# Performance work log

Hardware: AMD Instinct MI355X
Metric: run time of the kernel (lower is better)

The kernel has to match this reference:

```python
import jax, jax.numpy as jnp
import numpy as np

B, T, N, C = 32, 12, 2048, 1
D, K, H = 10, 2, 32


def setup_inputs() -> dict:
    key = jax.random.key(0)
    ks = jax.random.split(key, 8)
    s = 0.1  # small init scale for params
    return {
        "source": jax.random.normal(ks[0], (B, T, N, C), jnp.float32),
        "node_emb": jax.random.normal(ks[1], (N, D), jnp.float32),
        "gate_W": jax.random.normal(ks[2], (D, K, C + H, 2 * H), jnp.float32) * s,
        "gate_b": jax.random.normal(ks[3], (D, 2 * H), jnp.float32) * s,
        "upd_W": jax.random.normal(ks[4], (D, K, C + H, H), jnp.float32) * s,
        "upd_b": jax.random.normal(ks[5], (D, H), jnp.float32) * s,
        "conv_W": jax.random.normal(ks[6], (T * C, 1, 1, H), jnp.float32) * s,
        "conv_b": jax.random.normal(ks[7], (T * C,), jnp.float32) * s,
    }


def reference(source, node_emb, gate_W, gate_b, upd_W, upd_b, conv_W, conv_b):
    b, t, n, c = source.shape
    h = upd_W.shape[-1]
    k = gate_W.shape[1]
    dt = source.dtype
    E = node_emb

    # Adaptive adjacency from node embeddings (time-invariant -> hoist out of scan)
    A = jax.nn.softmax(jax.nn.relu(E @ E.T), axis=1)  # [N,N]
    sup = [jnp.eye(n, dtype=dt), A]
    for i in range(2, k):
        sup.append(2.0 * (A @ sup[-1]) - sup[-2])  # Chebyshev recursion
    S = jnp.stack(sup, 0)  # [K,N,N]

    # Node-specific weights/biases from embedding pools (also time-invariant)
    Wg = jnp.einsum('nd,dkio->nkio', E, gate_W)
    bg = E @ gate_b
    Wu = jnp.einsum('nd,dkio->nkio', E, upd_W)
    bu = E @ upd_b

    def gconv(x, W, bias):  # x: [B,N,Cin] -> [B,N,Cout]
        xg = jnp.einsum('knm,bmc->bnkc', S, x)
        return jnp.einsum('bnki,nkio->bno', xg, W) + bias

    def step(state, xt):  # GRU-style AGCRN cell
        xs = jnp.concatenate([xt, state], axis=-1)
        zr = jax.nn.sigmoid(gconv(xs, Wg, bg))
        z, r = jnp.split(zr, 2, axis=-1)
        hc = jnp.tanh(gconv(jnp.concatenate([xt, z * state], axis=-1), Wu, bu))
        hnew = r * state + (1.0 - r) * hc
        return hnew, None

    h0 = jnp.zeros((b, n, h), dtype=dt)
    h_last, _ = jax.lax.scan(step, h0, jnp.swapaxes(source, 0, 1))  # carry = last state

    # end_conv: Conv2d(1, T*C, kernel=(1,H)) on [B,1,N,H] == matmul over H
    out = jnp.einsum('bnh,oh->bon', h_last, conv_W[:, 0, 0, :]) + conv_b[None, :, None]
    out = out.reshape(b, t, c, n).transpose(0, 2, 3, 1)  # [B, C, N, T]
    return out
```

## Files before the change

### kernel.cpp

```cpp
#include <hip/hip_runtime.h>
#include <hip/hip_bf16.h>
#include <math.h>


#define NNODE 2048
#define NB 32
#define NT 12
#define NH 32
#define ND 10
#define NCOL 1024
#define NCX 384
#define KPAD 96
#define GPAD 104
#define WPAD 98

#define ASCALE 256.0f
#define AINV 0.00390625f

#define KSPLIT 4
#define KCHUNK 512
#define Y1S ((size_t)NNODE * NCOL)
#define AXPS ((size_t)NNODE * NCX)

typedef _Float16 half8 __attribute__((ext_vector_type(8)));
typedef float floatx4 __attribute__((ext_vector_type(4)));

#define AS1 __attribute__((address_space(1)))
#define AS3 __attribute__((address_space(3)))
__device__ __forceinline__ void gload16(const _Float16* g, _Float16* l) {
    __builtin_amdgcn_global_load_lds((const AS1 unsigned int*)(g),
                                     (AS3 unsigned int*)(l), 16, 0, 0);
}

constexpr size_t OFF_AH  = 0;
constexpr size_t OFF_WGT = OFF_AH + 2097152u;
constexpr size_t OFF_WUT = OFF_WGT + 6291456u;
constexpr size_t OFF_BG  = OFF_WUT + 3145728u;
constexpr size_t OFF_BU  = OFF_BG + 131072u;
constexpr size_t OFF_XT  = OFF_BU + 65536u;
constexpr size_t OFF_X2T = OFF_XT + 1048576u;
constexpr size_t OFF_SXT = OFF_X2T + 1048576u;
constexpr size_t OFF_HS  = OFF_SXT + 393216u;
constexpr size_t OFF_Y   = OFF_HS + 2097152u;
constexpr size_t OFF_AXP = OFF_Y + 4194304u;
constexpr size_t OFF_R   = OFF_AXP + 1572864u;
constexpr size_t OFF_ZH  = OFF_R + 1048576u;

__global__ __launch_bounds__(256) void adj_kernel(const float* __restrict__ E,
                                                  _Float16* __restrict__ Ah) {
    __shared__ float En[ND];
    __shared__ float red[256];
    const int n = blockIdx.x;
    const int t = threadIdx.x;
    if (t < ND) En[t] = E[n * ND + t];
    __syncthreads();
    float v[8];
    float mx = 0.f;
#pragma unroll
    for (int i = 0; i < 8; ++i) {
        const int m = t + i * 256;
        float acc = 0.f;
#pragma unroll
        for (int d = 0; d < ND; ++d) acc += En[d] * E[m * ND + d];
        acc = fmaxf(acc, 0.f);
        v[i] = acc;
        mx = fmaxf(mx, acc);
    }
    red[t] = mx;
    __syncthreads();
    for (int s = 128; s > 0; s >>= 1) {
        if (t < s) red[t] = fmaxf(red[t], red[t + s]);
        __syncthreads();
    }
    mx = red[0];
    __syncthreads();
    float sum = 0.f;
#pragma unroll
    for (int i = 0; i < 8; ++i) {
        v[i] = expf(v[i] - mx);
        sum += v[i];
    }
    red[t] = sum;
    __syncthreads();
    for (int s = 128; s > 0; s >>= 1) {
        if (t < s) red[t] += red[t + s];
        __syncthreads();
    }
    const float inv = ASCALE / red[0];
#pragma unroll
    for (int i = 0; i < 8; ++i)
        Ah[(size_t)n * NNODE + t + i * 256] = (_Float16)(v[i] * inv);
}

__global__ __launch_bounds__(256) void wg_kernel(const float* __restrict__ E,
                                                 const float* __restrict__ gW,
                                                 _Float16* __restrict__ Wgt) {
    __shared__ float Es[ND];
    __shared__ _Float16 Wl[64 * WPAD];
    const int n = blockIdx.x, t = threadIdx.x;
    if (t < ND) Es[t] = E[n * ND + t];
    for (int i = t; i < 64 * WPAD / 2; i += 256) ((unsigned*)Wl)[i] = 0u;
    __syncthreads();
    for (int rem = t; rem < 4224; rem += 256) {
        float acc = 0.f;
#pragma unroll
        for (int d = 0; d < ND; ++d) acc += Es[d] * gW[d * 4224 + rem];
        const int kk = rem / 2112, r2 = rem % 2112;
        const int i = r2 >> 6, o = r2 & 63;
        Wl[o * WPAD + kk * 33 + i] = (_Float16)acc;
    }
    __syncthreads();
    const unsigned* wl = (const unsigned*)Wl;
    unsigned* dst = (unsigned*)(Wgt + (size_t)n * 6144);
    for (int idx = t; idx < 64 * 48; idx += 256) {
        const int o = idx / 48, j = idx % 48;
        dst[idx] = wl[o * (WPAD / 2) + j];
    }
}

__global__ __launch_bounds__(256) void wu_kernel(const float* __restrict__ E,
                                                 const float* __restrict__ uW,
                                                 _Float16* __restrict__ Wut) {
    __shared__ float Es[ND];
    __shared__ _Float16 Wl[32 * WPAD];
    const int n = blockIdx.x, t = threadIdx.x;
    if (t < ND) Es[t] = E[n * ND + t];
    for (int i = t; i < 32 * WPAD / 2; i += 256) ((unsigned*)Wl)[i] = 0u;
    __syncthreads();
    for (int rem = t; rem < 2112; rem += 256) {
        float acc = 0.f;
#pragma unroll
        for (int d = 0; d < ND; ++d) acc += Es[d] * uW[d * 2112 + rem];
        const int kk = rem / 1056, r2 = rem % 1056;
        const int i = r2 >> 5, o = r2 & 31;
        Wl[o * WPAD + kk * 33 + i] = (_Float16)acc;
    }
    __syncthreads();
    const unsigned* wl = (const unsigned*)Wl;
    unsigned* dst = (unsigned*)(Wut + (size_t)n * 3072);
    for (int idx = t; idx < 32 * 48; idx += 256) {
        const int o = idx / 48, j = idx % 48;
        dst[idx] = wl[o * (WPAD / 2) + j];
    }
}

__global__ __launch_bounds__(256) void bias_kernel(const float* __restrict__ E,
                                                   const float* __restrict__ gb,
                                                   const float* __restrict__ ub,
                                                   float* __restrict__ bg,
                                                   float* __restrict__ bu) {
    const int idx = blockIdx.x * 256 + threadIdx.x;
    if (idx < NNODE * 64) {
        const int n = idx >> 6, o = idx & 63;
        float acc = 0.f;
#pragma unroll
        for (int d = 0; d < ND; ++d) acc += E[n * ND + d] * gb[d * 64 + o];
        bg[idx] = acc;
    } else if (idx < NNODE * 64 + NNODE * 32) {
        const int j = idx - NNODE * 64;
        const int n = j >> 5, o = j & 31;
        float acc = 0.f;
#pragma unroll
        for (int d = 0; d < ND; ++d) acc += E[n * ND + d] * ub[d * 32 + o];
        bu[j] = acc;
    }
}

__global__ __launch_bounds__(256) void setup_kernel(const float* __restrict__ src,
                                                    _Float16* __restrict__ XT,
                                                    _Float16* __restrict__ X2T,
                                                    _Float16* __restrict__ SXT,
                                                    float* __restrict__ Hs) {
    const int idx = blockIdx.x * 256 + threadIdx.x;
    XT[idx] = (_Float16)0.f;
    X2T[idx] = (_Float16)0.f;
    Hs[idx] = 0.f;
    if (idx < NCX * NNODE) {
        const int col = idx / NNODE, n = idx % NNODE;
        const int tt = col >> 5, b = col & 31;
        SXT[idx] = (_Float16)src[((size_t)b * NT + tt) * NNODE + n];
    }
}

__global__ __launch_bounds__(256) void mm_kernel(const _Float16* __restrict__ Ah,
                                                 const _Float16* __restrict__ XT,
                                                 _Float16* __restrict__ Y, int nct) {
    __shared__ _Float16 As[128 * 32];
    __shared__ _Float16 Bs[128 * 32];
    const int t = threadIdx.x;
    const int bid = blockIdx.x;
    const int xcd = bid & 7;
    const int kz = xcd >> 1;
    const int s = (bid >> 3) * 2 + (xcd & 1);
    const int m0 = (s & 15) * 128;
    const int c0 = (s >> 4) * 128;
    const int ncols = nct << 7;
    _Float16* __restrict__ Yp = Y + (size_t)kz * NNODE * ncols;
    const int lane = t & 63;
    const int w = t >> 6;
    const int wm = (w & 1) * 64;
    const int wn = (w >> 1) * 64;
    const int lm = lane & 15;
    const int q = lane >> 4;

    const int srow = w * 32 + (lane >> 2);
    const int sq = (lane & 3) ^ ((lane >> 3) & 3);
    const _Float16* gA = Ah + (size_t)(m0 + srow) * NNODE + kz * KCHUNK + sq * 8;
    const _Float16* gB = XT + (size_t)(c0 + srow) * NNODE + kz * KCHUNK + sq * 8;
    _Float16* lA = As + w * 1024;
    _Float16* lB = Bs + w * 1024;

    const int fp = (q ^ ((lm >> 1) & 3)) * 8;

    floatx4 acc[4][4] = {};

    for (int kt = 0; kt < KCHUNK; kt += 32) {
        gload16(gA, lA);
        gload16(gA + 16 * NNODE, lA + 512);
        gload16(gB, lB);
        gload16(gB + 16 * NNODE, lB + 512);
        gA += 32;
        gB += 32;
        __syncthreads();
        half8 af[4], bf[4];
#pragma unroll
        for (int mt = 0; mt < 4; ++mt)
            af[mt] = *(const half8*)&As[(wm + mt * 16 + lm) * 32 + fp];
#pragma unroll
        for (int nt = 0; nt < 4; ++nt)
            bf[nt] = *(const half8*)&Bs[(wn + nt * 16 + lm) * 32 + fp];
#pragma unroll
        for (int mt = 0; mt < 4; ++mt)
#pragma unroll
            for (int nt = 0; nt < 4; ++nt)
                acc[mt][nt] = __builtin_amdgcn_mfma_f32_16x16x32_f16(
                    af[mt], bf[nt], acc[mt][nt], 0, 0, 0);
        __syncthreads();
    }
#pragma unroll
    for (int mt = 0; mt < 4; ++mt) {
#pragma unroll
        for (int nt = 0; nt < 4; ++nt) {
            const int row = m0 + wm + mt * 16 + q * 4;
            const int col = c0 + wn + nt * 16 + lm;
#pragma unroll
            for (int r = 0; r < 4; ++r)
                Yp[(size_t)(row + r) * ncols + col] = (_Float16)(acc[mt][nt][r] * AINV);
        }
    }
}

__global__ __launch_bounds__(256) void gate_kernel(const float* __restrict__ src, int tcur,
                                                   const _Float16* __restrict__ Y,
                                                   const _Float16* __restrict__ AXP,
                                                   const _Float16* __restrict__ Wgt,
                                                   const float* __restrict__ bg,
                                                   const float* __restrict__ Hs,
                                                   _Float16* __restrict__ X2T,
                                                   _Float16* __restrict__ zh,
                                                   _Float16* __restrict__ rbuf) {
    __shared__ _Float16 catL[4][32][GPAD];
    const int t = threadIdx.x;
    const int n0 = blockIdx.x * 4;
    {
        const int pair = t >> 1, which = t & 1;
        const int nd = pair >> 5, b = pair & 31;
        const int n1 = n0 + nd;
        if (which == 0) {
            catL[nd][b][0] = (_Float16)src[((size_t)b * NT + tcur) * NNODE + n1];
            const float* hp = Hs + (size_t)n1 * 1024 + b * 32;
#pragma unroll
            for (int i = 0; i < 32; ++i) catL[nd][b][1 + i] = (_Float16)hp[i];
#pragma unroll
            for (int i = 66; i < KPAD; i += 2) *(unsigned*)&catL[nd][b][i] = 0u;
        } else {
            const _Float16* ax = AXP + (size_t)n1 * NCX + tcur * 32 + b;
            catL[nd][b][33] = (_Float16)((float)ax[0] + (float)ax[AXPS] +
                                         (float)ax[2 * AXPS] + (float)ax[3 * AXPS]);
            const _Float16* yp = Y + (size_t)n1 * NCOL + b * 32;
#pragma unroll
            for (int i = 0; i < 32; ++i) {
                const float sv = (float)yp[i] + (float)yp[Y1S + i] +
                                 (float)yp[2 * Y1S + i] + (float)yp[3 * Y1S + i];
                catL[nd][b][34 + i] = (_Float16)sv;
            }
        }
    }
    __syncthreads();
    const int w = t >> 6, lane = t & 63, lm = lane & 15, q = lane >> 4;
    const int n = n0 + w;
    const _Float16* Wn = Wgt + (size_t)n * 6144;
    floatx4 acc[2][4] = {};
#pragma unroll
    for (int kt = 0; kt < 3; ++kt) {
        half8 af[2], bf[4];
#pragma unroll
        for (int mt = 0; mt < 2; ++mt)
            af[mt] = *(const half8*)&catL[w][mt * 16 + lm][kt * 32 + q * 8];
#pragma unroll
        for (int nt = 0; nt < 4; ++nt)
            bf[nt] = *(const half8*)(Wn + (nt * 16 + lm) * KPAD + kt * 32 + q * 8);
#pragma unroll
        for (int mt = 0; mt < 2; ++mt)
#pragma unroll
            for (int nt = 0; nt < 4; ++nt)
                acc[mt][nt] = __builtin_amdgcn_mfma_f32_16x16x32_f16(
                    af[mt], bf[nt], acc[mt][nt], 0, 0, 0);
    }
#pragma unroll
    for (int nt = 0; nt < 4; ++nt) {
        const int o = nt * 16 + lm;
        const float bias = bg[n * 64 + o];
#pragma unroll
        for (int mt = 0; mt < 2; ++mt) {
#pragma unroll
            for (int r = 0; r < 4; ++r) {
                const int b = mt * 16 + q * 4 + r;
                const float s = 1.f / (1.f + expf(-(acc[mt][nt][r] + bias)));
                if (o < 32) {
                    const float hold = Hs[(size_t)n * 1024 + b * 32 + o];
                    const _Float16 zv = (_Float16)(s * hold);
                    zh[(size_t)n * 1024 + b * 32 + o] = zv;
                    X2T[(size_t)(b * 32 + o) * NNODE + n] = zv;
                } else {
                    rbuf[(size_t)n * 1024 + b * 32 + (o - 32)] = (_Float16)s;
                }
            }
        }
    }
}

__global__ __launch_bounds__(256) void upd_kernel(const float* __restrict__ src, int tcur,
                                                  const _Float16* __restrict__ Y,
                                                  const _Float16* __restrict__ AXP,
                                                  const _Float16* __restrict__ Wut,
                                                  const float* __restrict__ bu,
                                                  const _Float16* __restrict__ zh,
                                                  const _Float16* __restrict__ rbuf,
                                                  float* __restrict__ Hs,
                                                  _Float16* __restrict__ XT) {
    __shared__ _Float16 catL[4][32][GPAD];
    const int t = threadIdx.x;
    const int n0 = blockIdx.x * 4;
    {
        const int pair = t >> 1, which = t & 1;
        const int nd = pair >> 5, b = pair & 31;
        const int n1 = n0 + nd;
        if (which == 0) {
            catL[nd][b][0] = (_Float16)src[((size_t)b * NT + tcur) * NNODE + n1];
            const _Float16* zp = zh + (size_t)n1 * 1024 + b * 32;
#pragma unroll
            for (int i = 0; i < 32; ++i) catL[nd][b][1 + i] = zp[i];
#pragma unroll
            for (int i = 66; i < KPAD; i += 2) *(unsigned*)&catL[nd][b][i] = 0u;
        } else {
            const _Float16* ax = AXP + (size_t)n1 * NCX + tcur * 32 + b;
            catL[nd][b][33] = (_Float16)((float)ax[0] + (float)ax[AXPS] +
                                         (float)ax[2 * AXPS] + (float)ax[3 * AXPS]);
            const _Float16* yp = Y + (size_t)n1 * NCOL + b * 32;
#pragma unroll
            for (int i = 0; i < 32; ++i) {
                const float sv = (float)yp[i] + (float)yp[Y1S + i] +
                                 (float)yp[2 * Y1S + i] + (float)yp[3 * Y1S + i];
                catL[nd][b][34 + i] = (_Float16)sv;
            }
        }
    }
    __syncthreads();
    const int w = t >> 6, lane = t & 63, lm = lane & 15, q = lane >> 4;
    const int n = n0 + w;
    const _Float16* Wn = Wut + (size_t)n * 3072;
    floatx4 acc[2][2] = {};
#pragma unroll
    for (int kt = 0; kt < 3; ++kt) {
        half8 af[2], bf[2];
#pragma unroll
        for (int mt = 0; mt < 2; ++mt)
            af[mt] = *(const half8*)&catL[w][mt * 16 + lm][kt * 32 + q * 8];
#pragma unroll
        for (int nt = 0; nt < 2; ++nt)
            bf[nt] = *(const half8*)(Wn + (nt * 16 + lm) * KPAD + kt * 32 + q * 8);
#pragma unroll
        for (int mt = 0; mt < 2; ++mt)
#pragma unroll
            for (int nt = 0; nt < 2; ++nt)
                acc[mt][nt] = __builtin_amdgcn_mfma_f32_16x16x32_f16(
                    af[mt], bf[nt], acc[mt][nt], 0, 0, 0);
    }
#pragma unroll
    for (int nt = 0; nt < 2; ++nt) {
        const int o = nt * 16 + lm;
        const float bias = bu[n * 32 + o];
#pragma unroll
        for (int mt = 0; mt < 2; ++mt) {
#pragma unroll
            for (int r = 0; r < 4; ++r) {
                const int b = mt * 16 + q * 4 + r;
                const float hc = tanhf(acc[mt][nt][r] + bias);
                const float rr = (float)rbuf[(size_t)n * 1024 + b * 32 + o];
                const size_t hidx = (size_t)n * 1024 + b * 32 + o;
                const float hnew = rr * Hs[hidx] + (1.f - rr) * hc;
                Hs[hidx] = hnew;
                XT[(size_t)(b * 32 + o) * NNODE + n] = (_Float16)hnew;
            }
        }
    }
}

__global__ __launch_bounds__(256) void out_kernel(const float* __restrict__ Hs,
                                                  const float* __restrict__ cw,
                                                  const float* __restrict__ cb,
                                                  float* __restrict__ out) {
    __shared__ float h[NB * NH];
    __shared__ float cws[NT * NH];
    __shared__ float cbs[NT];
    const int n = blockIdx.x;
    const int t = threadIdx.x;
    for (int i = t; i < NT * NH; i += 256) cws[i] = cw[i];
    if (t < NT) cbs[t] = cb[t];
    for (int i = t; i < NB * NH; i += 256) h[i] = Hs[(size_t)n * 1024 + i];
    __syncthreads();
    for (int p = t; p < NB * NT; p += 256) {
        const int b = p / NT, tt = p % NT;
        float acc = cbs[tt];
#pragma unroll
        for (int j = 0; j < NH; ++j) acc += h[b * NH + j] * cws[tt * NH + j];
        out[(size_t)b * NNODE * NT + (size_t)n * NT + tt] = acc;
    }
}

extern "C" void kernel_launch(void* const* d_in, const int* in_sizes, int n_in,
                              void* d_out, int out_size, void* d_ws, size_t ws_size,
                              hipStream_t stream) {
    const float* src  = (const float*)d_in[0];
    const float* E    = (const float*)d_in[1];
    const float* gW   = (const float*)d_in[2];
    const float* gb   = (const float*)d_in[3];
    const float* uW   = (const float*)d_in[4];
    const float* ub   = (const float*)d_in[5];
    const float* cw   = (const float*)d_in[6];
    const float* cb   = (const float*)d_in[7];
    float* out = (float*)d_out;

    float* ws = (float*)d_ws;
    _Float16* Ah  = (_Float16*)(ws + OFF_AH);
    _Float16* Wgt = (_Float16*)(ws + OFF_WGT);
    _Float16* Wut = (_Float16*)(ws + OFF_WUT);
    float* bg  = ws + OFF_BG;
    float* bu  = ws + OFF_BU;
    _Float16* XT  = (_Float16*)(ws + OFF_XT);
    _Float16* X2T = (_Float16*)(ws + OFF_X2T);
    _Float16* SXT = (_Float16*)(ws + OFF_SXT);
    float* Hs  = ws + OFF_HS;
    _Float16* Y   = (_Float16*)(ws + OFF_Y);
    _Float16* AXP = (_Float16*)(ws + OFF_AXP);
    _Float16* rb  = (_Float16*)(ws + OFF_R);
    _Float16* zh  = (_Float16*)(ws + OFF_ZH);

    adj_kernel<<<NNODE, 256, 0, stream>>>(E, Ah);
    wg_kernel<<<NNODE, 256, 0, stream>>>(E, gW, Wgt);
    wu_kernel<<<NNODE, 256, 0, stream>>>(E, uW, Wut);
    bias_kernel<<<(NNODE * 96 + 255) / 256, 256, 0, stream>>>(E, gb, ub, bg, bu);
    setup_kernel<<<NNODE * NCOL / 256, 256, 0, stream>>>(src, XT, X2T, SXT, Hs);

    mm_kernel<<<64 * 3, 256, 0, stream>>>(Ah, SXT, AXP, 3);

    for (int t = 0; t < NT; ++t) {
        mm_kernel<<<64 * 8, 256, 0, stream>>>(Ah, XT, Y, 8);
        gate_kernel<<<NNODE / 4, 256, 0, stream>>>(src, t, Y, AXP, Wgt, bg, Hs, X2T, zh, rb);
        mm_kernel<<<64 * 8, 256, 0, stream>>>(Ah, X2T, Y, 8);
        upd_kernel<<<NNODE / 4, 256, 0, stream>>>(src, t, Y, AXP, Wut, bu, zh, rb, Hs, XT);
    }
    out_kernel<<<NNODE, 256, 0, stream>>>(Hs, cw, cb, out);
}
```

Measured before the change: 1.167 ms.

## Fuse preprocessing kernels into one launch and deepen mm K-tile to 64

Merges the five setup kernels (adjacency softmax, gate/update weight generation, biases, buffer init) into a single block-indexed pre_kernel to cut launch overhead. The adjacency matmul kernel now stages 64-wide K tiles with an XOR swizzle over 8 chunks, halving the number of barrier/load iterations per K chunk. This doubles LDS per mm block, which may reduce occupancy.

After: 1.109 ms. 1.05x faster.

```diff
diff --git a/kernel.cpp b/kernel.cpp
--- a/kernel.cpp
+++ b/kernel.cpp
@@ -1,7 +1,6 @@
 #include <hip/hip_runtime.h>
 #include <hip/hip_bf16.h>
 #include <math.h>
-
 
 #define NNODE 2048
 #define NB 32
@@ -17,7 +16,6 @@
 #define ASCALE 256.0f
 #define AINV 0.00390625f
 
-#define KSPLIT 4
 #define KCHUNK 512
 #define Y1S ((size_t)NNODE * NCOL)
 #define AXPS ((size_t)NNODE * NCX)
@@ -46,147 +44,138 @@
 constexpr size_t OFF_R   = OFF_AXP + 1572864u;
 constexpr size_t OFF_ZH  = OFF_R + 1048576u;
 
-__global__ __launch_bounds__(256) void adj_kernel(const float* __restrict__ E,
-                                                  _Float16* __restrict__ Ah) {
-    __shared__ float En[ND];
-    __shared__ float red[256];
-    const int n = blockIdx.x;
+__global__ __launch_bounds__(256) void pre_kernel(
+    const float* __restrict__ E, const float* __restrict__ gW,
+    const float* __restrict__ uW, const float* __restrict__ gb,
+    const float* __restrict__ ub, const float* __restrict__ src,
+    _Float16* __restrict__ Ah, _Float16* __restrict__ Wgt,
+    _Float16* __restrict__ Wut, float* __restrict__ bg, float* __restrict__ bu,
+    _Float16* __restrict__ XT, _Float16* __restrict__ X2T,
+    _Float16* __restrict__ SXT, float* __restrict__ Hs) {
+    __shared__ __align__(16) float pre_f[3168];
+    const int bidg = blockIdx.x;
     const int t = threadIdx.x;
-    if (t < ND) En[t] = E[n * ND + t];
-    __syncthreads();
-    float v[8];
-    float mx = 0.f;
-#pragma unroll
-    for (int i = 0; i < 8; ++i) {
-        const int m = t + i * 256;
-        float acc = 0.f;
-#pragma unroll
-        for (int d = 0; d < ND; ++d) acc += En[d] * E[m * ND + d];
-        acc = fmaxf(acc, 0.f);
-        v[i] = acc;
-        mx = fmaxf(mx, acc);
-    }
-    red[t] = mx;
-    __syncthreads();
-    for (int s = 128; s > 0; s >>= 1) {
-        if (t < s) red[t] = fmaxf(red[t], red[t + s]);
-        __syncthreads();
-    }
-    mx = red[0];
-    __syncthreads();
-    float sum = 0.f;
-#pragma unroll
-    for (int i = 0; i < 8; ++i) {
-        v[i] = expf(v[i] - mx);
-        sum += v[i];
-    }
-    red[t] = sum;
-    __syncthreads();
-    for (int s = 128; s > 0; s >>= 1) {
-        if (t < s) red[t] += red[t + s];
-        __syncthreads();
-    }
-    const float inv = ASCALE / red[0];
-#pragma unroll
-    for (int i = 0; i < 8; ++i)
-        Ah[(size_t)n * NNODE + t + i * 256] = (_Float16)(v[i] * inv);
-}
-
-__global__ __launch_bounds__(256) void wg_kernel(const float* __restrict__ E,
-                                                 const float* __restrict__ gW,
-                                                 _Float16* __restrict__ Wgt) {
-    __shared__ float Es[ND];
-    __shared__ _Float16 Wl[64 * WPAD];
-    const int n = blockIdx.x, t = threadIdx.x;
-    if (t < ND) Es[t] = E[n * ND + t];
-    for (int i = t; i < 64 * WPAD / 2; i += 256) ((unsigned*)Wl)[i] = 0u;
-    __syncthreads();
-    for (int rem = t; rem < 4224; rem += 256) {
-        float acc = 0.f;
-#pragma unroll
-        for (int d = 0; d < ND; ++d) acc += Es[d] * gW[d * 4224 + rem];
-        const int kk = rem / 2112, r2 = rem % 2112;
-        const int i = r2 >> 6, o = r2 & 63;
-        Wl[o * WPAD + kk * 33 + i] = (_Float16)acc;
-    }
-    __syncthreads();
-    const unsigned* wl = (const unsigned*)Wl;
-    unsigned* dst = (unsigned*)(Wgt + (size_t)n * 6144);
-    for (int idx = t; idx < 64 * 48; idx += 256) {
-        const int o = idx / 48, j = idx % 48;
-        dst[idx] = wl[o * (WPAD / 2) + j];
-    }
-}
-
-__global__ __launch_bounds__(256) void wu_kernel(const float* __restrict__ E,
-                                                 const float* __restrict__ uW,
-                                                 _Float16* __restrict__ Wut) {
-    __shared__ float Es[ND];
-    __shared__ _Float16 Wl[32 * WPAD];
-    const int n = blockIdx.x, t = threadIdx.x;
-    if (t < ND) Es[t] = E[n * ND + t];
-    for (int i = t; i < 32 * WPAD / 2; i += 256) ((unsigned*)Wl)[i] = 0u;
-    __syncthreads();
-    for (int rem = t; rem < 2112; rem += 256) {
-        float acc = 0.f;
-#pragma unroll
-        for (int d = 0; d < ND; ++d) acc += Es[d] * uW[d * 2112 + rem];
-        const int kk = rem / 1056, r2 = rem % 1056;
-        const int i = r2 >> 5, o = r2 & 31;
-        Wl[o * WPAD + kk * 33 + i] = (_Float16)acc;
-    }
-    __syncthreads();
-    const unsigned* wl = (const unsigned*)Wl;
-    unsigned* dst = (unsigned*)(Wut + (size_t)n * 3072);
-    for (int idx = t; idx < 32 * 48; idx += 256) {
-        const int o = idx / 48, j = idx % 48;
-        dst[idx] = wl[o * (WPAD / 2) + j];
-    }
-}
-
-__global__ __launch_bounds__(256) void bias_kernel(const float* __restrict__ E,
-                                                   const float* __restrict__ gb,
-                                                   const float* __restrict__ ub,
-                                                   float* __restrict__ bg,
-                                                   float* __restrict__ bu) {
-    const int idx = blockIdx.x * 256 + threadIdx.x;
-    if (idx < NNODE * 64) {
-        const int n = idx >> 6, o = idx & 63;
-        float acc = 0.f;
-#pragma unroll
-        for (int d = 0; d < ND; ++d) acc += E[n * ND + d] * gb[d * 64 + o];
-        bg[idx] = acc;
-    } else if (idx < NNODE * 64 + NNODE * 32) {
-        const int j = idx - NNODE * 64;
-        const int n = j >> 5, o = j & 31;
-        float acc = 0.f;
-#pragma unroll
-        for (int d = 0; d < ND; ++d) acc += E[n * ND + d] * ub[d * 32 + o];
-        bu[j] = acc;
-    }
-}
-
-__global__ __launch_bounds__(256) void setup_kernel(const float* __restrict__ src,
-                                                    _Float16* __restrict__ XT,
-                                                    _Float16* __restrict__ X2T,
-                                                    _Float16* __restrict__ SXT,
-                                                    float* __restrict__ Hs) {
-    const int idx = blockIdx.x * 256 + threadIdx.x;
-    XT[idx] = (_Float16)0.f;
-    X2T[idx] = (_Float16)0.f;
-    Hs[idx] = 0.f;
-    if (idx < NCX * NNODE) {
-        const int col = idx / NNODE, n = idx % NNODE;
-        const int tt = col >> 5, b = col & 31;
-        SXT[idx] = (_Float16)src[((size_t)b * NT + tt) * NNODE + n];
+
+    if (bidg < 2048) {
+        float* En = pre_f;
+        float* red = pre_f + 16;
+        const int n = bidg;
+        if (t < ND) En[t] = E[n * ND + t];
+        __syncthreads();
+        float v[8];
+        float mx = 0.f;
+#pragma unroll
+        for (int i = 0; i < 8; ++i) {
+            const int m = t + i * 256;
+            float acc = 0.f;
+#pragma unroll
+            for (int d = 0; d < ND; ++d) acc += En[d] * E[m * ND + d];
+            acc = fmaxf(acc, 0.f);
+            v[i] = acc;
+            mx = fmaxf(mx, acc);
+        }
+        red[t] = mx;
+        __syncthreads();
+        for (int s = 128; s > 0; s >>= 1) {
+            if (t < s) red[t] = fmaxf(red[t], red[t + s]);
+            __syncthreads();
+        }
+        mx = red[0];
+        __syncthreads();
+        float sum = 0.f;
+#pragma unroll
+        for (int i = 0; i < 8; ++i) {
+            v[i] = expf(v[i] - mx);
+            sum += v[i];
+        }
+        red[t] = sum;
+        __syncthreads();
+        for (int s = 128; s > 0; s >>= 1) {
+            if (t < s) red[t] += red[t + s];
+            __syncthreads();
+        }
+        const float inv = ASCALE / red[0];
+#pragma unroll
+        for (int i = 0; i < 8; ++i)
+            Ah[(size_t)n * NNODE + t + i * 256] = (_Float16)(v[i] * inv);
+    } else if (bidg < 4096) {
+        float* Es = pre_f;
+        _Float16* Wl = (_Float16*)(pre_f + 16);
+        const int n = bidg - 2048;
+        if (t < ND) Es[t] = E[n * ND + t];
+        for (int i = t; i < 64 * WPAD / 2; i += 256) ((unsigned*)Wl)[i] = 0u;
+        __syncthreads();
+        for (int rem = t; rem < 4224; rem += 256) {
+            float acc = 0.f;
+#pragma unroll
+            for (int d = 0; d < ND; ++d) acc += Es[d] * gW[d * 4224 + rem];
+            const int kk = rem / 2112, r2 = rem % 2112;
+            const int i = r2 >> 6, o = r2 & 63;
+            Wl[o * WPAD + kk * 33 + i] = (_Float16)acc;
+        }
+        __syncthreads();
+        const unsigned* wl = (const unsigned*)Wl;
+        unsigned* dst = (unsigned*)(Wgt + (size_t)n * 6144);
+        for (int idx = t; idx < 64 * 48; idx += 256) {
+            const int o = idx / 48, j = idx % 48;
+            dst[idx] = wl[o * (WPAD / 2) + j];
+        }
+    } else if (bidg < 6144) {
+        float* Es = pre_f;
+        _Float16* Wl = (_Float16*)(pre_f + 16);
+        const int n = bidg - 4096;
+        if (t < ND) Es[t] = E[n * ND + t];
+        for (int i = t; i < 32 * WPAD / 2; i += 256) ((unsigned*)Wl)[i] = 0u;
+        __syncthreads();
+        for (int rem = t; rem < 2112; rem += 256) {
+            float acc = 0.f;
+#pragma unroll
+            for (int d = 0; d < ND; ++d) acc += Es[d] * uW[d * 2112 + rem];
+            const int kk = rem / 1056, r2 = rem % 1056;
+            const int i = r2 >> 5, o = r2 & 31;
+            Wl[o * WPAD + kk * 33 + i] = (_Float16)acc;
+        }
+        __syncthreads();
+        const unsigned* wl = (const unsigned*)Wl;
+        unsigned* dst = (unsigned*)(Wut + (size_t)n * 3072);
+        for (int idx = t; idx < 32 * 48; idx += 256) {
+            const int o = idx / 48, j = idx % 48;
+            dst[idx] = wl[o * (WPAD / 2) + j];
+        }
+    } else if (bidg < 6912) {
+        const int idx = (bidg - 6144) * 256 + t;
+        if (idx < NNODE * 64) {
+            const int n = idx >> 6, o = idx & 63;
+            float acc = 0.f;
+#pragma unroll
+            for (int d = 0; d < ND; ++d) acc += E[n * ND + d] * gb[d * 64 + o];
+            bg[idx] = acc;
+        } else {
+            const int j = idx - NNODE * 64;
+            const int n = j >> 5, o = j & 31;
+            float acc = 0.f;
+#pragma unroll
+            for (int d = 0; d < ND; ++d) acc += E[n * ND + d] * ub[d * 32 + o];
+            bu[j] = acc;
+        }
+    } else {
+        const int idx = (bidg - 6912) * 256 + t;
+        XT[idx] = (_Float16)0.f;
+        X2T[idx] = (_Float16)0.f;
+        Hs[idx] = 0.f;
+        if (idx < NCX * NNODE) {
+            const int col = idx >> 11, n = idx & 2047;
+            const int tt = col >> 5, b = col & 31;
+            SXT[idx] = (_Float16)src[((size_t)b * NT + tt) * NNODE + n];
+        }
     }
 }
 
 __global__ __launch_bounds__(256) void mm_kernel(const _Float16* __restrict__ Ah,
                                                  const _Float16* __restrict__ XT,
                                                  _Float16* __restrict__ Y, int nct) {
-    __shared__ _Float16 As[128 * 32];
-    __shared__ _Float16 Bs[128 * 32];
+    __shared__ _Float16 As[128 * 64];
+    __shared__ _Float16 Bs[128 * 64];
     const int t = threadIdx.x;
     const int bid = blockIdx.x;
     const int xcd = bid & 7;
@@ -203,38 +192,41 @@
     const int lm = lane & 15;
     const int q = lane >> 4;
 
-    const int srow = w * 32 + (lane >> 2);
-    const int sq = (lane & 3) ^ ((lane >> 3) & 3);
-    const _Float16* gA = Ah + (size_t)(m0 + srow) * NNODE + kz * KCHUNK + sq * 8;
-    const _Float16* gB = XT + (size_t)(c0 + srow) * NNODE + kz * KCHUNK + sq * 8;
-    _Float16* lA = As + w * 1024;
-    _Float16* lB = Bs + w * 1024;
-
-    const int fp = (q ^ ((lm >> 1) & 3)) * 8;
+    const int srow = w * 32 + (lane >> 3);
+    const int sc = ((lane & 7) ^ (lane >> 3)) * 8;
+    const _Float16* gA = Ah + (size_t)(m0 + srow) * NNODE + kz * KCHUNK + sc;
+    const _Float16* gB = XT + (size_t)(c0 + srow) * NNODE + kz * KCHUNK + sc;
+    _Float16* lA = As + w * 2048;
+    _Float16* lB = Bs + w * 2048;
 
     floatx4 acc[4][4] = {};
 
-    for (int kt = 0; kt < KCHUNK; kt += 32) {
-        gload16(gA, lA);
-        gload16(gA + 16 * NNODE, lA + 512);
-        gload16(gB, lB);
-        gload16(gB + 16 * NNODE, lB + 512);
-        gA += 32;
-        gB += 32;
-        __syncthreads();
-        half8 af[4], bf[4];
-#pragma unroll
-        for (int mt = 0; mt < 4; ++mt)
-            af[mt] = *(const half8*)&As[(wm + mt * 16 + lm) * 32 + fp];
-#pragma unroll
-        for (int nt = 0; nt < 4; ++nt)
-            bf[nt] = *(const half8*)&Bs[(wn + nt * 16 + lm) * 32 + fp];
-#pragma unroll
-        for (int mt = 0; mt < 4; ++mt)
+    for (int kt = 0; kt < KCHUNK; kt += 64) {
+#pragma unroll
+        for (int j = 0; j < 4; ++j) {
+            gload16(gA + (size_t)j * 8 * NNODE, lA + j * 512);
+            gload16(gB + (size_t)j * 8 * NNODE, lB + j * 512);
+        }
+        gA += 64;
+        gB += 64;
+        __syncthreads();
+#pragma unroll
+        for (int ks = 0; ks < 2; ++ks) {
+            const int pc = ((ks * 4 + q) ^ (lm & 7)) * 8;
+            half8 af[4], bf[4];
+#pragma unroll
+            for (int mt = 0; mt < 4; ++mt)
+                af[mt] = *(const half8*)&As[(wm + mt * 16 + lm) * 64 + pc];
 #pragma unroll
             for (int nt = 0; nt < 4; ++nt)
-                acc[mt][nt] = __builtin_amdgcn_mfma_f32_16x16x32_f16(
-                    af[mt], bf[nt], acc[mt][nt], 0, 0, 0);
+                bf[nt] = *(const half8*)&Bs[(wn + nt * 16 + lm) * 64 + pc];
+#pragma unroll
+            for (int mt = 0; mt < 4; ++mt)
+#pragma unroll
+                for (int nt = 0; nt < 4; ++nt)
+                    acc[mt][nt] = __builtin_amdgcn_mfma_f32_16x16x32_f16(
+                        af[mt], bf[nt], acc[mt][nt], 0, 0, 0);
+        }
         __syncthreads();
     }
 #pragma unroll
@@ -249,6 +241,8 @@
         }
     }
 }
+
+#define CAT(nd, b, i) cat[((nd) * 32 + (b)) * GPAD + (i)]
 
 __global__ __launch_bounds__(256) void gate_kernel(const float* __restrict__ src, int tcur,
                                                    const _Float16* __restrict__ Y,
@@ -259,7 +253,7 @@
                                                    _Float16* __restrict__ X2T,
                                                    _Float16* __restrict__ zh,
                                                    _Float16* __restrict__ rbuf) {
-    __shared__ _Float16 catL[4][32][GPAD];
+    __shared__ __align__(16) _Float16 cat[4 * 32 * GPAD];
     const int t = threadIdx.x;
     const int n0 = blockIdx.x * 4;
     {
@@ -267,22 +261,22 @@
         const int nd = pair >> 5, b = pair & 31;
         const int n1 = n0 + nd;
         if (which == 0) {
-            catL[nd][b][0] = (_Float16)src[((size_t)b * NT + tcur) * NNODE + n1];
+            CAT(nd, b, 0) = (_Float16)src[((size_t)b * NT + tcur) * NNODE + n1];
             const float* hp = Hs + (size_t)n1 * 1024 + b * 32;
 #pragma unroll
-            for (int i = 0; i < 32; ++i) catL[nd][b][1 + i] = (_Float16)hp[i];
-#pragma unroll
-            for (int i = 66; i < KPAD; i += 2) *(unsigned*)&catL[nd][b][i] = 0u;
+            for (int i = 0; i < 32; ++i) CAT(nd, b, 1 + i) = (_Float16)hp[i];
+#pragma unroll
+            for (int i = 66; i < KPAD; i += 2) *(unsigned*)&CAT(nd, b, i) = 0u;
         } else {
             const _Float16* ax = AXP + (size_t)n1 * NCX + tcur * 32 + b;
-            catL[nd][b][33] = (_Float16)((float)ax[0] + (float)ax[AXPS] +
-                                         (float)ax[2 * AXPS] + (float)ax[3 * AXPS]);
+            CAT(nd, b, 33) = (_Float16)((float)ax[0] + (float)ax[AXPS] +
+                                        (float)ax[2 * AXPS] + (float)ax[3 * AXPS]);
             const _Float16* yp = Y + (size_t)n1 * NCOL + b * 32;
 #pragma unroll
             for (int i = 0; i < 32; ++i) {
                 const float sv = (float)yp[i] + (float)yp[Y1S + i] +
                                  (float)yp[2 * Y1S + i] + (float)yp[3 * Y1S + i];
-                catL[nd][b][34 + i] = (_Float16)sv;
+                CAT(nd, b, 34 + i) = (_Float16)sv;
             }
         }
     }
@@ -296,7 +290,7 @@
         half8 af[2], bf[4];
 #pragma unroll
         for (int mt = 0; mt < 2; ++mt)
-            af[mt] = *(const half8*)&catL[w][mt * 16 + lm][kt * 32 + q * 8];
+            af[mt] = *(const half8*)&CAT(w, mt * 16 + lm, kt * 32 + q * 8);
 #pragma unroll
         for (int nt = 0; nt < 4; ++nt)
             bf[nt] = *(const half8*)(Wn + (nt * 16 + lm) * KPAD + kt * 32 + q * 8);
@@ -339,7 +333,7 @@
                                                   const _Float16* __restrict__ rbuf,
                                                   float* __restrict__ Hs,
                                                   _Float16* __restrict__ XT) {
-    __shared__ _Float16 catL[4][32][GPAD];
+    __shared__ __align__(16) _Float16 cat[4 * 32 * GPAD];
     const int t = threadIdx.x;
     const int n0 = blockIdx.x * 4;
     {
@@ -347,22 +341,22 @@
         const int nd = pair >> 5, b = pair & 31;
         const int n1 = n0 + nd;
         if (which == 0) {
-            catL[nd][b][0] = (_Float16)src[((size_t)b * NT + tcur) * NNODE + n1];
+            CAT(nd, b, 0) = (_Float16)src[((size_t)b * NT + tcur) * NNODE + n1];
             const _Float16* zp = zh + (size_t)n1 * 1024 + b * 32;
 #pragma unroll
-            for (int i = 0; i < 32; ++i) catL[nd][b][1 + i] = zp[i];
-#pragma unroll
-            for (int i = 66; i < KPAD; i += 2) *(unsigned*)&catL[nd][b][i] = 0u;
+            for (int i = 0; i < 32; ++i) CAT(nd, b, 1 + i) = zp[i];
+#pragma unroll
+            for (int i = 66; i < KPAD; i += 2) *(unsigned*)&CAT(nd, b, i) = 0u;
         } else {
             const _Float16* ax = AXP + (size_t)n1 * NCX + tcur * 32 + b;
-            catL[nd][b][33] = (_Float16)((float)ax[0] + (float)ax[AXPS] +
-                                         (float)ax[2 * AXPS] + (float)ax[3 * AXPS]);
+            CAT(nd, b, 33) = (_Float16)((float)ax[0] + (float)ax[AXPS] +
+                                        (float)ax[2 * AXPS] + (float)ax[3 * AXPS]);
             const _Float16* yp = Y + (size_t)n1 * NCOL + b * 32;
 #pragma unroll
             for (int i = 0; i < 32; ++i) {
                 const float sv = (float)yp[i] + (float)yp[Y1S + i] +
                                  (float)yp[2 * Y1S + i] + (float)yp[3 * Y1S + i];
-                catL[nd][b][34 + i] = (_Float16)sv;
+                CAT(nd, b, 34 + i) = (_Float16)sv;
             }
         }
     }
@@ -376,7 +370,7 @@
         half8 af[2], bf[2];
 #pragma unroll
         for (int mt = 0; mt < 2; ++mt)
-            af[mt] = *(const half8*)&catL[w][mt * 16 + lm][kt * 32 + q * 8];
+            af[mt] = *(const half8*)&CAT(w, mt * 16 + lm, kt * 32 + q * 8);
 #pragma unroll
         for (int nt = 0; nt < 2; ++nt)
             bf[nt] = *(const half8*)(Wn + (nt * 16 + lm) * KPAD + kt * 32 + q * 8);
@@ -457,11 +451,8 @@
     _Float16* rb  = (_Float16*)(ws + OFF_R);
     _Float16* zh  = (_Float16*)(ws + OFF_ZH);
 
-    adj_kernel<<<NNODE, 256, 0, stream>>>(E, Ah);
-    wg_kernel<<<NNODE, 256, 0, stream>>>(E, gW, Wgt);
-    wu_kernel<<<NNODE, 256, 0, stream>>>(E, uW, Wut);
-    bias_kernel<<<(NNODE * 96 + 255) / 256, 256, 0, stream>>>(E, gb, ub, bg, bu);
-    setup_kernel<<<NNODE * NCOL / 256, 256, 0, stream>>>(src, XT, X2T, SXT, Hs);
+    pre_kernel<<<15104, 256, 0, stream>>>(E, gW, uW, gb, ub, src,
+                                          Ah, Wgt, Wut, bg, bu, XT, X2T, SXT, Hs);
 
     mm_kernel<<<64 * 3, 256, 0, stream>>>(Ah, SXT, AXP, 3);
 
```
